# Kernel optimization log

Measured on AMD Instinct MI355X. Metric: run time of the kernel, lower is better.

The kernel has to match this reference:

```python
import jax, jax.numpy as jnp
import numpy as np

B, S, HID = 8, 4096, 4096
NH, HD, ROT = 32, 128, 64  # heads, head_dim, rotary_dim (rotary_percentage=0.5)
FFN = 16384
EPS = 1e-5
SCALE = HD ** -0.5


def _ln1p(x, w, b):
    # LayerNorm1P: layer_norm with (weight + 1)
    mu = jnp.mean(x, axis=-1, keepdims=True)
    var = jnp.var(x, axis=-1, keepdims=True)
    return (x - mu) * jax.lax.rsqrt(var + EPS) * (w + 1.0) + b


def _rope(x, pos):
    # x: [B, NH, ROT] (rotary slice), pos: [B] int. GPT-NeoX style (rotate halves).
    half = ROT // 2
    inv_freq = 1.0 / (10000.0 ** (jnp.arange(0, ROT, 2, dtype=jnp.float32) / ROT))
    ang = pos[:, None].astype(jnp.float32) * inv_freq       # [B, half]
    cos = jnp.cos(ang)[:, None, :].astype(x.dtype)           # [B, 1, half]
    sin = jnp.sin(ang)[:, None, :].astype(x.dtype)
    x1, x2 = x[..., :half], x[..., half:]
    return jnp.concatenate([x1 * cos - x2 * sin, x2 * cos + x1 * sin], axis=-1)


def setup_inputs() -> dict:
    key = jax.random.key(0)
    ks = jax.random.split(key, 12)
    w = lambda k, shp: (jax.random.normal(k, shp, jnp.float32) * 0.02)
    return {
        "hidden_states": jax.random.normal(ks[0], (B, HID), jnp.float32),
        "k_cache": jax.random.normal(ks[1], (B, S, NH, HD), jnp.float32),
        "v_cache": jax.random.normal(ks[2], (B, S, NH, HD), jnp.float32),
        "w_qkv": w(ks[3], (HID, 3 * HID)),
        "w_dense": w(ks[4], (HID, HID)),
        "w_fc1": w(ks[5], (HID, 2 * FFN)),
        "w_fc2": w(ks[6], (FFN, HID)),
        "ln1_w": jax.random.normal(ks[7], (HID,), jnp.float32) * 0.02,
        "ln1_b": jnp.zeros((HID,), jnp.float32),
        "ln2_w": jax.random.normal(ks[8], (HID,), jnp.float32) * 0.02,
        "ln2_b": jnp.zeros((HID,), jnp.float32),
        "positions": jax.random.randint(ks[9], (B,), 0, S, jnp.int64),
    }


def reference(hidden_states, k_cache, v_cache, w_qkv, w_dense, w_fc1, w_fc2,
              ln1_w, ln1_b, ln2_w, ln2_b, positions):
    residual = hidden_states
    x = _ln1p(hidden_states, ln1_w, ln1_b)

    # fused QKV projection, chunk along last dim
    qkv = x @ w_qkv                                          # [B, 3*HID]
    q, k, v = jnp.split(qkv, 3, axis=-1)
    q = q.reshape(B, NH, HD)
    k = k.reshape(B, NH, HD)
    v = v.reshape(B, NH, HD)

    # inline RoPE on first ROT dims of q and new k
    q = jnp.concatenate([_rope(q[..., :ROT], positions), q[..., ROT:]], axis=-1)
    k = jnp.concatenate([_rope(k[..., :ROT], positions), k[..., ROT:]], axis=-1)

    # write new token's k/v into the paged KV cache at its slot
    bidx = jnp.arange(B)
    k_cache = k_cache.at[bidx, positions].set(k)
    v_cache = v_cache.at[bidx, positions].set(v)

    # single-query paged attention over cached keys, causal to current position
    scores = jnp.einsum('bhd,bshd->bhs', q, k_cache) * SCALE  # [B, NH, S]
    valid = jnp.arange(S)[None, None, :] <= positions[:, None, None]
    scores = jnp.where(valid, scores, jnp.finfo(scores.dtype).min)
    probs = jax.nn.softmax(scores, axis=-1)
    attn = jnp.einsum('bhs,bshd->bhd', probs, v_cache).reshape(B, HID)

    hidden_states = residual + attn @ w_dense

    residual = hidden_states
    x = _ln1p(hidden_states, ln2_w, ln2_b)
    h = x @ w_fc1                                            # [B, 2*FFN]
    h1, h2 = jnp.split(h, 2, axis=-1)
    x = (jax.nn.silu(h1) * h2) @ w_fc2                       # SwiGLU
    return residual + x
```

## Files before the change

### kernel.cpp

```cpp
#include <hip/hip_runtime.h>
#include <cstddef>
#include <cstdint>

#define NB 8
#define SEQ 4096
#define HIDDIM 4096
#define NHEAD 32
#define HDIM 128
#define FFNDIM 16384
#define ATTN_SCALE 0.08838834764831845f

__device__ __forceinline__ float wave_sum(float v) {
#pragma unroll
  for (int off = 32; off > 0; off >>= 1) v += __shfl_xor(v, off, 64);
  return v;
}

__device__ __forceinline__ int get_pos(const int* __restrict__ p, int b) {
  const bool is64 = ((p[1] | p[3] | p[5] | p[7]) == 0);
  return is64 ? p[2 * b] : p[b];
}

__global__ __launch_bounds__(256) void ln_rows(const float* __restrict__ in,
                                               const float* __restrict__ w,
                                               const float* __restrict__ bias,
                                               float* __restrict__ out_t) {
  __shared__ float row[HIDDIM];
  __shared__ float red[4];
  const int b = blockIdx.x, t = threadIdx.x;
  float s = 0.f;
  for (int i = t; i < HIDDIM; i += 256) {
    const float v = in[(size_t)b * HIDDIM + i];
    row[i] = v;
    s += v;
  }
  s = wave_sum(s);
  if ((t & 63) == 0) red[t >> 6] = s;
  __syncthreads();
  const float mean = (red[0] + red[1] + red[2] + red[3]) * (1.0f / HIDDIM);
  __syncthreads();
  float vs = 0.f;
  for (int i = t; i < HIDDIM; i += 256) {
    const float d = row[i] - mean;
    vs += d * d;
  }
  vs = wave_sum(vs);
  if ((t & 63) == 0) red[t >> 6] = vs;
  __syncthreads();
  const float var = (red[0] + red[1] + red[2] + red[3]) * (1.0f / HIDDIM);
  const float rs = rsqrtf(var + 1e-5f);
  for (int i = t; i < HIDDIM; i += 256) {
    out_t[(size_t)i * NB + b] = (row[i] - mean) * rs * (w[i] + 1.0f) + bias[i];
  }
}

template <int KCHUNK>
__global__ __launch_bounds__(256) void gemm8(const float* __restrict__ W,
                                             const float* __restrict__ xt,
                                             float* __restrict__ part, int N) {
  const int j0 = (blockIdx.x * 256 + threadIdx.x) * 4;
  const size_t i0 = (size_t)blockIdx.y * KCHUNK;
  const float* __restrict__ wp = W + i0 * N + j0;
  const float* __restrict__ xp = xt + i0 * NB;
  float4 a0 = {0, 0, 0, 0}, a1 = {0, 0, 0, 0}, a2 = {0, 0, 0, 0}, a3 = {0, 0, 0, 0};
  float4 a4 = {0, 0, 0, 0}, a5 = {0, 0, 0, 0}, a6 = {0, 0, 0, 0}, a7 = {0, 0, 0, 0};
#pragma unroll 4
  for (int i = 0; i < KCHUNK; ++i) {
    const float4 w = *reinterpret_cast<const float4*>(wp + (size_t)i * N);
    const float4 xa = *reinterpret_cast<const float4*>(xp + i * NB);
    const float4 xb = *reinterpret_cast<const float4*>(xp + i * NB + 4);
#define ACC4(A, sxx)                                                          \
  A.x = fmaf(sxx, w.x, A.x);                                                  \
  A.y = fmaf(sxx, w.y, A.y);                                                  \
  A.z = fmaf(sxx, w.z, A.z);                                                  \
  A.w = fmaf(sxx, w.w, A.w);
    ACC4(a0, xa.x) ACC4(a1, xa.y) ACC4(a2, xa.z) ACC4(a3, xa.w)
    ACC4(a4, xb.x) ACC4(a5, xb.y) ACC4(a6, xb.z) ACC4(a7, xb.w)
#undef ACC4
  }
  float* op = part + (size_t)blockIdx.y * NB * N + j0;
  *reinterpret_cast<float4*>(op) = a0; op += N;
  *reinterpret_cast<float4*>(op) = a1; op += N;
  *reinterpret_cast<float4*>(op) = a2; op += N;
  *reinterpret_cast<float4*>(op) = a3; op += N;
  *reinterpret_cast<float4*>(op) = a4; op += N;
  *reinterpret_cast<float4*>(op) = a5; op += N;
  *reinterpret_cast<float4*>(op) = a6; op += N;
  *reinterpret_cast<float4*>(op) = a7;
}

__global__ __launch_bounds__(128) void rope_reduce(const float* __restrict__ part, int nchunk,
                                                   const int* __restrict__ posp,
                                                   float* __restrict__ qo,
                                                   float* __restrict__ ko,
                                                   float* __restrict__ vo) {
  const int blk = blockIdx.x;
  const int b = blk >> 5, h = blk & 31;
  const int d = threadIdx.x;
  const int col = h * HDIM + d;
  float qs = 0.f, ks = 0.f, vs = 0.f;
  for (int c = 0; c < nchunk; ++c) {
    const float* p = part + ((size_t)c * NB + b) * (3 * HIDDIM);
    qs += p[col];
    ks += p[HIDDIM + col];
    vs += p[2 * HIDDIM + col];
  }
  __shared__ float qsh[HDIM], ksh[HDIM];
  qsh[d] = qs;
  ksh[d] = ks;
  __syncthreads();
  float qv = qs, kv = ks;
  if (d < 64) {
    const int f = d & 31;
    const float ang = (float)get_pos(posp, b) * powf(10000.0f, -(float)f * (1.0f / 32.0f));
    const float cs = cosf(ang), sn = sinf(ang);
    if (d < 32) {
      qv = qsh[d] * cs - qsh[d + 32] * sn;
      kv = ksh[d] * cs - ksh[d + 32] * sn;
    } else {
      qv = qsh[d] * cs + qsh[d - 32] * sn;
      kv = ksh[d] * cs + ksh[d - 32] * sn;
    }
  }
  qo[(size_t)b * HIDDIM + col] = qv;
  ko[(size_t)b * HIDDIM + col] = kv;
  vo[(size_t)b * HIDDIM + col] = vs;
}

__global__ __launch_bounds__(256) void attn_split(
    const float* __restrict__ kc, const float* __restrict__ vc,
    const float* __restrict__ q, const float* __restrict__ kn,
    const float* __restrict__ vn, const int* __restrict__ posp,
    float* __restrict__ Mp, float* __restrict__ Lp, float* __restrict__ Ap) {
  const int c = blockIdx.x, h = blockIdx.y, b = blockIdx.z;
  const int pos = get_pos(posp, b);
  const int s0 = c * 256;
  if (s0 > pos) return;
  const int s1 = min(s0 + 256, pos + 1);
  const int wid = threadIdx.x >> 6, lane = threadIdx.x & 63;
  const int dd = 2 * lane;
  const float2 qv = *reinterpret_cast<const float2*>(q + (size_t)b * HIDDIM + h * HDIM + dd);
  const float* kb = kc + ((size_t)b * SEQ * NHEAD + h) * HDIM + dd;
  const float* vb = vc + ((size_t)b * SEQ * NHEAD + h) * HDIM + dd;
  const float* knp = kn + (size_t)b * HIDDIM + h * HDIM + dd;
  const float* vnp = vn + (size_t)b * HIDDIM + h * HDIM + dd;
  float m = -INFINITY, l = 0.f;
  float2 acc = {0.f, 0.f};
  for (int s = s0 + wid; s < s1; s += 4) {
    const float* kp = (s == pos) ? knp : kb + (size_t)s * (NHEAD * HDIM);
    const float* vp = (s == pos) ? vnp : vb + (size_t)s * (NHEAD * HDIM);
    const float2 kk = *reinterpret_cast<const float2*>(kp);
    const float2 vv = *reinterpret_cast<const float2*>(vp);
    float p = qv.x * kk.x + qv.y * kk.y;
    p = wave_sum(p) * ATTN_SCALE;
    const float mn = fmaxf(m, p);
    const float cf = __expf(m - mn);
    const float pw = __expf(p - mn);
    l = l * cf + pw;
    acc.x = acc.x * cf + pw * vv.x;
    acc.y = acc.y * cf + pw * vv.y;
    m = mn;
  }
  __shared__ float sm[4], sl[4], sa[4][HDIM];
  sa[wid][dd] = acc.x;
  sa[wid][dd + 1] = acc.y;
  if (lane == 0) { sm[wid] = m; sl[wid] = l; }
  __syncthreads();
  if (threadIdx.x < HDIM) {
    const int d = threadIdx.x;
    const float M = fmaxf(fmaxf(sm[0], sm[1]), fmaxf(sm[2], sm[3]));
    float L = 0.f, A = 0.f;
#pragma unroll
    for (int w2 = 0; w2 < 4; ++w2) {
      const float e = __expf(sm[w2] - M);
      L += e * sl[w2];
      A += e * sa[w2][d];
    }
    const size_t idx = (size_t)(b * NHEAD + h) * 16 + c;
    if (d == 0) { Mp[idx] = M; Lp[idx] = L; }
    Ap[idx * HDIM + d] = A;
  }
}

__global__ __launch_bounds__(128) void attn_combine(
    const float* __restrict__ Mp, const float* __restrict__ Lp,
    const float* __restrict__ Ap, const int* __restrict__ posp,
    float* __restrict__ out_t) {
  const int blk = blockIdx.x;
  const int b = blk >> 5, h = blk & 31;
  const int d = threadIdx.x;
  const int nc = get_pos(posp, b) / 256 + 1;
  const size_t base = (size_t)(b * NHEAD + h) * 16;
  float M = -INFINITY;
  for (int c = 0; c < nc; ++c) M = fmaxf(M, Mp[base + c]);
  float L = 0.f, A = 0.f;
  for (int c = 0; c < nc; ++c) {
    const float e = __expf(Mp[base + c] - M);
    L += e * Lp[base + c];
    A += e * Ap[(base + c) * HDIM + d];
  }
  out_t[(size_t)(h * HDIM + d) * NB + b] = A / L;
}

__global__ __launch_bounds__(256) void reduce_add(const float* __restrict__ part, int nchunk,
                                                  const float* __restrict__ base,
                                                  float* __restrict__ out) {
  const int idx = blockIdx.x * 256 + threadIdx.x;
  float v = base[idx];
  for (int c = 0; c < nchunk; ++c) v += part[(size_t)c * (NB * HIDDIM) + idx];
  out[idx] = v;
}

__global__ __launch_bounds__(256) void gate_silu(const float* __restrict__ part, int nchunk,
                                                 float* __restrict__ gt) {
  const int j = blockIdx.x * 256 + threadIdx.x;
  const int b = blockIdx.y;
  float h1 = 0.f, h2 = 0.f;
  for (int c = 0; c < nchunk; ++c) {
    const float* p = part + ((size_t)c * NB + b) * (2 * FFNDIM);
    h1 += p[j];
    h2 += p[FFNDIM + j];
  }
  const float g = (h1 / (1.f + __expf(-h1))) * h2;
  gt[(size_t)j * NB + b] = g;
}

extern "C" void kernel_launch(void* const* d_in, const int* in_sizes, int n_in,
                              void* d_out, int out_size, void* d_ws, size_t ws_size,
                              hipStream_t stream) {
  const float* hs = (const float*)d_in[0];
  const float* kc = (const float*)d_in[1];
  const float* vc = (const float*)d_in[2];
  const float* wqkv = (const float*)d_in[3];
  const float* wdense = (const float*)d_in[4];
  const float* wfc1 = (const float*)d_in[5];
  const float* wfc2 = (const float*)d_in[6];
  const float* ln1w = (const float*)d_in[7];
  const float* ln1b = (const float*)d_in[8];
  const float* ln2w = (const float*)d_in[9];
  const float* ln2b = (const float*)d_in[10];
  const int* posp = (const int*)d_in[11];
  float* out = (float*)d_out;

  float* ws = (float*)d_ws;
  float* x1t = ws;
  float* qws = x1t + 32768;
  float* kws = qws + 32768;
  float* vws = kws + 32768;
  float* attnt = vws + 32768;
  float* hidden2 = attnt + 32768;
  float* x2t = hidden2 + 32768;
  float* gt = x2t + 32768;
  float* Mp = gt + 131072;
  float* Lp = Mp + 4096;
  float* Ap = Lp + 4096;
  float* part = Ap + 524288;

  ln_rows<<<8, 256, 0, stream>>>(hs, ln1w, ln1b, x1t);
  gemm8<128><<<dim3(12, 32), 256, 0, stream>>>(wqkv, x1t, part, 3 * HIDDIM);
  rope_reduce<<<256, 128, 0, stream>>>(part, 32, posp, qws, kws, vws);
  attn_split<<<dim3(16, NHEAD, NB), 256, 0, stream>>>(kc, vc, qws, kws, vws, posp, Mp, Lp, Ap);
  attn_combine<<<256, 128, 0, stream>>>(Mp, Lp, Ap, posp, attnt);
  gemm8<128><<<dim3(4, 32), 256, 0, stream>>>(wdense, attnt, part, HIDDIM);
  reduce_add<<<128, 256, 0, stream>>>(part, 32, hs, hidden2);
  ln_rows<<<8, 256, 0, stream>>>(hidden2, ln2w, ln2b, x2t);
  gemm8<256><<<dim3(32, 16), 256, 0, stream>>>(wfc1, x2t, part, 2 * FFNDIM);
  gate_silu<<<dim3(64, NB), 256, 0, stream>>>(part, 16, gt);
  gemm8<256><<<dim3(4, 64), 256, 0, stream>>>(wfc2, gt, part, HIDDIM);
  reduce_add<<<128, 256, 0, stream>>>(part, 64, hidden2, out);
}
```

Baseline: 416.0 us.

## Stage activations in LDS, widen attention lanes, and rebalance GEMM split-K

The GEMM kernel now copies its activation chunk into shared memory once per block and sets a 2-blocks occupancy hint. The attention split kernel processes two sequence positions per wave using float4 loads on half-waves, with 8 partial softmax states merged at the end. Split-K chunk sizes for the QKV, dense and fc2 GEMMs are reduced, which adds more blocks and more partial sums for the reduce kernels to read. The aim is more parallelism for weight streaming and wider KV-cache loads, at the cost of extra partial-sum traffic.

```diff
diff --git a/kernel.cpp b/kernel.cpp
--- a/kernel.cpp
+++ b/kernel.cpp
@@ -55,20 +55,27 @@
 }
 
 template <int KCHUNK>
-__global__ __launch_bounds__(256) void gemm8(const float* __restrict__ W,
-                                             const float* __restrict__ xt,
-                                             float* __restrict__ part, int N) {
-  const int j0 = (blockIdx.x * 256 + threadIdx.x) * 4;
+__global__ __launch_bounds__(256, 2) void gemm8(const float* __restrict__ W,
+                                                const float* __restrict__ xt,
+                                                float* __restrict__ part, int N) {
+  __shared__ float xs[KCHUNK * NB];
+  const int t = threadIdx.x;
   const size_t i0 = (size_t)blockIdx.y * KCHUNK;
+  {
+    const float4* src = reinterpret_cast<const float4*>(xt + i0 * NB);
+    float4* dst = reinterpret_cast<float4*>(xs);
+    for (int idx = t; idx < KCHUNK * NB / 4; idx += 256) dst[idx] = src[idx];
+  }
+  __syncthreads();
+  const int j0 = (blockIdx.x * 256 + t) * 4;
   const float* __restrict__ wp = W + i0 * N + j0;
-  const float* __restrict__ xp = xt + i0 * NB;
   float4 a0 = {0, 0, 0, 0}, a1 = {0, 0, 0, 0}, a2 = {0, 0, 0, 0}, a3 = {0, 0, 0, 0};
   float4 a4 = {0, 0, 0, 0}, a5 = {0, 0, 0, 0}, a6 = {0, 0, 0, 0}, a7 = {0, 0, 0, 0};
 #pragma unroll 4
   for (int i = 0; i < KCHUNK; ++i) {
     const float4 w = *reinterpret_cast<const float4*>(wp + (size_t)i * N);
-    const float4 xa = *reinterpret_cast<const float4*>(xp + i * NB);
-    const float4 xb = *reinterpret_cast<const float4*>(xp + i * NB + 4);
+    const float4 xa = *reinterpret_cast<const float4*>(xs + i * NB);
+    const float4 xb = *reinterpret_cast<const float4*>(xs + i * NB + 4);
 #define ACC4(A, sxx)                                                          \
   A.x = fmaf(sxx, w.x, A.x);                                                  \
   A.y = fmaf(sxx, w.y, A.y);                                                  \
@@ -138,40 +145,48 @@
   if (s0 > pos) return;
   const int s1 = min(s0 + 256, pos + 1);
   const int wid = threadIdx.x >> 6, lane = threadIdx.x & 63;
-  const int dd = 2 * lane;
-  const float2 qv = *reinterpret_cast<const float2*>(q + (size_t)b * HIDDIM + h * HDIM + dd);
-  const float* kb = kc + ((size_t)b * SEQ * NHEAD + h) * HDIM + dd;
-  const float* vb = vc + ((size_t)b * SEQ * NHEAD + h) * HDIM + dd;
-  const float* knp = kn + (size_t)b * HIDDIM + h * HDIM + dd;
-  const float* vnp = vn + (size_t)b * HIDDIM + h * HDIM + dd;
-  float m = -INFINITY, l = 0.f;
-  float2 acc = {0.f, 0.f};
-  for (int s = s0 + wid; s < s1; s += 4) {
+  const int half = lane >> 5;
+  const int d4 = (lane & 31) * 4;
+  const float4 qv = *reinterpret_cast<const float4*>(q + (size_t)b * HIDDIM + h * HDIM + d4);
+  const float* kb = kc + ((size_t)b * SEQ * NHEAD + h) * HDIM + d4;
+  const float* vb = vc + ((size_t)b * SEQ * NHEAD + h) * HDIM + d4;
+  const float* knp = kn + (size_t)b * HIDDIM + h * HDIM + d4;
+  const float* vnp = vn + (size_t)b * HIDDIM + h * HDIM + d4;
+  float m = -1e30f, l = 0.f;
+  float4 acc = {0.f, 0.f, 0.f, 0.f};
+  for (int sb = s0; sb < s1; sb += 8) {
+    const int s = sb + wid * 2 + half;
     const float* kp = (s == pos) ? knp : kb + (size_t)s * (NHEAD * HDIM);
     const float* vp = (s == pos) ? vnp : vb + (size_t)s * (NHEAD * HDIM);
-    const float2 kk = *reinterpret_cast<const float2*>(kp);
-    const float2 vv = *reinterpret_cast<const float2*>(vp);
-    float p = qv.x * kk.x + qv.y * kk.y;
-    p = wave_sum(p) * ATTN_SCALE;
+    const float4 kk = *reinterpret_cast<const float4*>(kp);
+    const float4 vv = *reinterpret_cast<const float4*>(vp);
+    float p = qv.x * kk.x + qv.y * kk.y + qv.z * kk.z + qv.w * kk.w;
+#pragma unroll
+    for (int off = 16; off > 0; off >>= 1) p += __shfl_xor(p, off, 64);
+    p = (s < s1) ? p * ATTN_SCALE : -2e30f;
     const float mn = fmaxf(m, p);
     const float cf = __expf(m - mn);
     const float pw = __expf(p - mn);
     l = l * cf + pw;
     acc.x = acc.x * cf + pw * vv.x;
     acc.y = acc.y * cf + pw * vv.y;
+    acc.z = acc.z * cf + pw * vv.z;
+    acc.w = acc.w * cf + pw * vv.w;
     m = mn;
   }
-  __shared__ float sm[4], sl[4], sa[4][HDIM];
-  sa[wid][dd] = acc.x;
-  sa[wid][dd + 1] = acc.y;
-  if (lane == 0) { sm[wid] = m; sl[wid] = l; }
+  __shared__ float sm[8], sl[8], sa[8][HDIM];
+  const int st = wid * 2 + half;
+  *reinterpret_cast<float4*>(&sa[st][d4]) = acc;
+  if ((lane & 31) == 0) { sm[st] = m; sl[st] = l; }
   __syncthreads();
   if (threadIdx.x < HDIM) {
     const int d = threadIdx.x;
-    const float M = fmaxf(fmaxf(sm[0], sm[1]), fmaxf(sm[2], sm[3]));
+    float M = -1e30f;
+#pragma unroll
+    for (int w2 = 0; w2 < 8; ++w2) M = fmaxf(M, sm[w2]);
     float L = 0.f, A = 0.f;
 #pragma unroll
-    for (int w2 = 0; w2 < 4; ++w2) {
+    for (int w2 = 0; w2 < 8; ++w2) {
       const float e = __expf(sm[w2] - M);
       L += e * sl[w2];
       A += e * sa[w2][d];
@@ -191,7 +206,7 @@
   const int d = threadIdx.x;
   const int nc = get_pos(posp, b) / 256 + 1;
   const size_t base = (size_t)(b * NHEAD + h) * 16;
-  float M = -INFINITY;
+  float M = -1e30f;
   for (int c = 0; c < nc; ++c) M = fmaxf(M, Mp[base + c]);
   float L = 0.f, A = 0.f;
   for (int c = 0; c < nc; ++c) {
@@ -202,10 +217,10 @@
   out_t[(size_t)(h * HDIM + d) * NB + b] = A / L;
 }
 
-__global__ __launch_bounds__(256) void reduce_add(const float* __restrict__ part, int nchunk,
+__global__ __launch_bounds__(128) void reduce_add(const float* __restrict__ part, int nchunk,
                                                   const float* __restrict__ base,
                                                   float* __restrict__ out) {
-  const int idx = blockIdx.x * 256 + threadIdx.x;
+  const int idx = blockIdx.x * 128 + threadIdx.x;
   float v = base[idx];
   for (int c = 0; c < nchunk; ++c) v += part[(size_t)c * (NB * HIDDIM) + idx];
   out[idx] = v;
@@ -257,15 +272,15 @@
   float* part = Ap + 524288;
 
   ln_rows<<<8, 256, 0, stream>>>(hs, ln1w, ln1b, x1t);
-  gemm8<128><<<dim3(12, 32), 256, 0, stream>>>(wqkv, x1t, part, 3 * HIDDIM);
-  rope_reduce<<<256, 128, 0, stream>>>(part, 32, posp, qws, kws, vws);
+  gemm8<64><<<dim3(12, 64), 256, 0, stream>>>(wqkv, x1t, part, 3 * HIDDIM);
+  rope_reduce<<<256, 128, 0, stream>>>(part, 64, posp, qws, kws, vws);
   attn_split<<<dim3(16, NHEAD, NB), 256, 0, stream>>>(kc, vc, qws, kws, vws, posp, Mp, Lp, Ap);
   attn_combine<<<256, 128, 0, stream>>>(Mp, Lp, Ap, posp, attnt);
-  gemm8<128><<<dim3(4, 32), 256, 0, stream>>>(wdense, attnt, part, HIDDIM);
-  reduce_add<<<128, 256, 0, stream>>>(part, 32, hs, hidden2);
+  gemm8<32><<<dim3(4, 128), 256, 0, stream>>>(wdense, attnt, part, HIDDIM);
+  reduce_add<<<256, 128, 0, stream>>>(part, 128, hs, hidden2);
   ln_rows<<<8, 256, 0, stream>>>(hidden2, ln2w, ln2b, x2t);
   gemm8<256><<<dim3(32, 16), 256, 0, stream>>>(wfc1, x2t, part, 2 * FFNDIM);
   gate_silu<<<dim3(64, NB), 256, 0, stream>>>(part, 16, gt);
-  gemm8<256><<<dim3(4, 64), 256, 0, stream>>>(wfc2, gt, part, HIDDIM);
-  reduce_add<<<128, 256, 0, stream>>>(part, 64, hidden2, out);
-}
+  gemm8<128><<<dim3(4, 128), 256, 0, stream>>>(wfc2, gt, part, HIDDIM);
+  reduce_add<<<256, 128, 0, stream>>>(part, 128, hidden2, out);
+}
```

After: 456.6 us. 9.8% more time.
